# Kernel optimization log

Hardware: AMD Instinct MI355X
Metric: run time of the kernel (lower is better)

## Reference

```python
import jax, jax.numpy as jnp
import numpy as np

N, G, NPG = 51200, 512, 100
E, FA, FE = 300000, 64, 8
H, NH, DH, L, T = 256, 8, 32, 4, 5


def setup_inputs() -> dict:
    key = jax.random.key(0)
    it = iter(jax.random.split(key, 40))
    def rn(shape, s=0.05):
        return jax.random.normal(next(it), shape, jnp.float32) * s
    inp = {
        "x": rn((N, FA), 1.0),
        "edge_attr": rn((E, FE), 1.0),
        "edge_index": jax.random.randint(next(it), (2, E), 0, N),
        "batch": jnp.repeat(jnp.arange(G), NPG),
        "atom_w": rn((FA, H)), "atom_b": jnp.zeros((H,), jnp.float32),
        "edge_w": rn((FE, H)), "edge_b": jnp.zeros((H,), jnp.float32),
        "gat_lin_w": rn((L, H, H)), "gat_lin_edge_w": rn((L, H, H)),
        "gat_att_src": rn((L, NH, DH)), "gat_att_dst": rn((L, NH, DH)), "gat_att_edge": rn((L, NH, DH)),
        "gat_bias": jnp.zeros((L, H), jnp.float32),
        "bn_gamma": jnp.ones((L, H), jnp.float32), "bn_beta": jnp.zeros((L, H), jnp.float32),
        "mha_in_w": rn((3 * H, H)), "mha_in_b": jnp.zeros((3 * H,), jnp.float32),
        "mha_out_w": rn((H, H)), "mha_out_b": jnp.zeros((H,), jnp.float32),
        "sh_w1": rn((H, H)), "sh_b1": jnp.zeros((H,), jnp.float32),
        "sh_w2": rn((H, H // 2)), "sh_b2": jnp.zeros((H // 2,), jnp.float32),
        "head_w1": rn((T, H // 2, H // 4)), "head_b1": jnp.zeros((T, H // 4), jnp.float32),
        "head_w2": rn((T, H // 4, 1)), "head_b2": jnp.zeros((T, 1), jnp.float32),
    }
    return inp


def _forward(x, edge_attr, edge_index, batch, atom_w, atom_b, edge_w, edge_b,
             gat_lin_w, gat_lin_edge_w, gat_att_src, gat_att_dst, gat_att_edge,
             gat_bias, bn_gamma, bn_beta, mha_in_w, mha_in_b, mha_out_w, mha_out_b,
             sh_w1, sh_b1, sh_w2, sh_b2, head_w1, head_b1, head_w2, head_b2):
    src, dst = edge_index[0], edge_index[1]
    h = x @ atom_w + atom_b                      # [N, H] atom_encoder
    e = edge_attr @ edge_w + edge_b              # [E, H] edge_encoder
    # PyG GATConv add_self_loops=True, fill_value='mean' for edge_attr
    deg = jax.ops.segment_sum(jnp.ones((E,), e.dtype), dst, num_segments=N)
    e_self = jax.ops.segment_sum(e, dst, num_segments=N) / jnp.maximum(deg, 1.0)[:, None]
    loop = jnp.arange(N)
    src_f = jnp.concatenate([src, loop])
    dst_f = jnp.concatenate([dst, loop])
    e_f = jnp.concatenate([e, e_self], axis=0)   # [E+N, H]
    for i in range(L):
        res = h
        xs = (h @ gat_lin_w[i]).reshape(N, NH, DH)
        a_src = (xs * gat_att_src[i]).sum(-1)    # [N, NH]
        a_dst = (xs * gat_att_dst[i]).sum(-1)
        ee = (e_f @ gat_lin_edge_w[i]).reshape(-1, NH, DH)
        a_e = (ee * gat_att_edge[i]).sum(-1)     # [E+N, NH]
        alpha = jax.nn.leaky_relu(a_src[src_f] + a_dst[dst_f] + a_e, 0.2)
        mx = jax.ops.segment_max(alpha, dst_f, num_segments=N)   # segment softmax over dst
        ex = jnp.exp(alpha - mx[dst_f])
        den = jax.ops.segment_sum(ex, dst_f, num_segments=N)
        w = ex / (den[dst_f] + 1e-16)            # [E+N, NH]
        out = jax.ops.segment_sum(xs[src_f] * w[..., None], dst_f, num_segments=N)
        out = out.reshape(N, H) + gat_bias[i]
        mu = out.mean(0)
        var = out.var(0)                         # training-mode BatchNorm
        out = bn_gamma[i] * (out - mu) * jax.lax.rsqrt(var + 1e-5) + bn_beta[i]
        h = jax.nn.relu(out)
        if i > 0:
            h = h + res
    # per-graph MHA: graphs are fixed-size, so the ragged loop == batched attention
    xg = h.reshape(G, NPG, H)
    qkv = xg @ mha_in_w.T + mha_in_b             # [G, n, 3H]
    q, k, v = jnp.split(qkv, 3, axis=-1)
    def heads(t):
        return t.reshape(G, NPG, NH, DH).transpose(0, 2, 1, 3)
    q = heads(q) * (1.0 / np.sqrt(DH))
    k, v = heads(k), heads(v)
    att = jax.nn.softmax(jnp.einsum("ghnd,ghmd->ghnm", q, k), axis=-1)
    o = jnp.einsum("ghnm,ghmd->ghnd", att, v).transpose(0, 2, 1, 3).reshape(G, NPG, H)
    o = o @ mha_out_w.T + mha_out_b
    pooled = o.mean(1)                           # [G, H]
    s = jax.nn.relu(pooled @ sh_w1 + sh_b1)
    s = jax.nn.relu(s @ sh_w2 + sh_b2)           # [G, H//2]
    hh = jax.nn.relu(jnp.einsum("gd,tdk->gtk", s, head_w1) + head_b1)
    pred = jnp.einsum("gtk,tko->gto", hh, head_w2)[..., 0] + head_b2[:, 0]
    return pred                                  # [G, T]


def reference(x, edge_attr, edge_index, batch, atom_w, atom_b, edge_w, edge_b,
              gat_lin_w, gat_lin_edge_w, gat_att_src, gat_att_dst, gat_att_edge,
              gat_bias, bn_gamma, bn_beta, mha_in_w, mha_in_b, mha_out_w, mha_out_b,
              sh_w1, sh_b1, sh_w2, sh_b2, head_w1, head_b1, head_w2, head_b2):
    return _forward(x, edge_attr, edge_index, batch, atom_w, atom_b, edge_w, edge_b,
                    gat_lin_w, gat_lin_edge_w, gat_att_src, gat_att_dst, gat_att_edge,
                    gat_bias, bn_gamma, bn_beta, mha_in_w, mha_in_b, mha_out_w, mha_out_b,
                    sh_w1, sh_b1, sh_w2, sh_b2, head_w1, head_b1, head_w2, head_b2)
```

## Files before the change

### kernel.cpp

```cpp
#include <hip/hip_runtime.h>
#include <hip/hip_bf16.h>

#define N_NODES 51200
#define N_EDGES 300000
#define NFULL   351200
#define GRAPHS  512
#define NPGRAPH 100
#define FATOM   64
#define FEDGE   8
#define HDIM    256
#define NHEADS  8
#define DHEAD   32
#define LAYERS  4
#define TASKS   5
#define BN_SLOTS 16
#define SCAN_BLOCKS 50

typedef unsigned short u16;
typedef __attribute__((ext_vector_type(8))) short bf16x8;
typedef __attribute__((ext_vector_type(4))) float f32x4;

__device__ __forceinline__ float b2f(u16 u) {
    return __uint_as_float(((unsigned)u) << 16);
}
__device__ __forceinline__ u16 f2bf(float f) {
    unsigned u = __float_as_uint(f);
    unsigned r = u + 0x7fffu + ((u >> 16) & 1u);
    return (u16)(r >> 16);
}

__global__ __launch_bounds__(256)
void convert_kernel(const float* __restrict__ in, u16* __restrict__ out, int n) {
    int i = blockIdx.x * 256 + threadIdx.x;
    if (i < n) out[i] = f2bf(in[i]);
}

__global__ __launch_bounds__(256)
void convert_t_kernel(const float* __restrict__ in, u16* __restrict__ out, int R, int C) {
    int idx = blockIdx.x * 256 + threadIdx.x;
    if (idx >= R * C) return;
    int c = idx / R, r = idx % R;
    out[idx] = f2bf(in[(size_t)r * C + c]);
}

__global__ __launch_bounds__(256)
void convert_t4_kernel(const float* __restrict__ in, u16* __restrict__ out) {
    int idx = blockIdx.x * 256 + threadIdx.x;
    int li = idx >> 16, rem = idx & 65535;
    int c = rem >> 8, r = rem & 255;
    out[idx] = f2bf(in[(size_t)li * 65536 + r * 256 + c]);
}

template<bool BIAS, bool RELU>
__global__ __launch_bounds__(256, 2)
void gemm_mfma_kernel(const u16* __restrict__ A, const u16* __restrict__ Bt,
                      const float* __restrict__ bias, u16* __restrict__ C,
                      int M, int K, int N) {
    __shared__ u16 smem[136 * 128];
    u16* As = smem;
    u16* Bs = smem + 128 * 64;
    const int t = threadIdx.x;
    const int lane = t & 63;
    const int w = t >> 6;
    const int wr = w >> 1, wc = w & 1;

    const int nwg = (int)gridDim.x;
    const int bid = (int)blockIdx.x;
    const int q = nwg >> 3, r = nwg & 7;
    const int xcd = bid & 7, idx0 = bid >> 3;
    const int wgid = (xcd < r) ? xcd * (q + 1) + idx0
                               : r * (q + 1) + (xcd - r) * q + idx0;
    const int nx = N >> 7;
    const int bn = (wgid % nx) * 128;
    const int bm = (wgid / nx) * 128;

    f32x4 acc[4][4] = {};

    for (int kt = 0; kt < K; kt += 64) {
        uint4 ra[4], rb[4];
#pragma unroll
        for (int i = 0; i < 4; ++i) {
            int idx = i * 256 + t;
            int row = idx >> 3, ch = idx & 7;
            ra[i] = *(const uint4*)(A + (size_t)(bm + row) * K + kt + ch * 8);
            rb[i] = *(const uint4*)(Bt + (size_t)(bn + row) * K + kt + ch * 8);
        }
        __syncthreads();
#pragma unroll
        for (int i = 0; i < 4; ++i) {
            int idx = i * 256 + t;
            int row = idx >> 3, ch = idx & 7;
            int sw = ch ^ (row & 7);
            *(uint4*)((char*)As + row * 128 + sw * 16) = ra[i];
            *(uint4*)((char*)Bs + row * 128 + sw * 16) = rb[i];
        }
        __syncthreads();
#pragma unroll
        for (int kk = 0; kk < 2; ++kk) {
            bf16x8 af[4], bf[4];
#pragma unroll
            for (int m = 0; m < 4; ++m) {
                int rr = wr * 64 + m * 16 + (lane & 15);
                int ch = kk * 4 + (lane >> 4);
                af[m] = *(const bf16x8*)((const char*)As + rr * 128 + ((ch ^ (rr & 7)) << 4));
            }
#pragma unroll
            for (int n = 0; n < 4; ++n) {
                int rr = wc * 64 + n * 16 + (lane & 15);
                int ch = kk * 4 + (lane >> 4);
                bf[n] = *(const bf16x8*)((const char*)Bs + rr * 128 + ((ch ^ (rr & 7)) << 4));
            }
#pragma unroll
            for (int m = 0; m < 4; ++m)
#pragma unroll
                for (int n = 0; n < 4; ++n)
                    acc[m][n] = __builtin_amdgcn_mfma_f32_16x16x32_bf16(
                        af[m], bf[n], acc[m][n], 0, 0, 0);
        }
    }
    __syncthreads();
#pragma unroll
    for (int m = 0; m < 4; ++m)
#pragma unroll
        for (int n = 0; n < 4; ++n) {
            int coll = wc * 64 + n * 16 + (lane & 15);
            float bv = BIAS ? bias[bn + coll] : 0.f;
#pragma unroll
            for (int j = 0; j < 4; ++j) {
                float v = acc[m][n][j] + bv;
                if (RELU) v = fmaxf(v, 0.f);
                int rowl = wr * 64 + m * 16 + (lane >> 4) * 4 + j;
                smem[rowl * 136 + coll] = f2bf(v);
            }
        }
    __syncthreads();
#pragma unroll
    for (int p = 0; p < 8; ++p) {
        int rowl = p * 16 + (t >> 4);
        uint4 v = *(const uint4*)(smem + rowl * 136 + (t & 15) * 8);
        *(uint4*)(C + (size_t)(bm + rowl) * N + bn + (t & 15) * 8) = v;
    }
}

__global__ __launch_bounds__(256)
void edge_hist_kernel(const int* __restrict__ dst, int* __restrict__ deg) {
    int e = blockIdx.x * 256 + threadIdx.x;
    if (e >= N_EDGES) return;
    atomicAdd(&deg[dst[e]], 1);
}

__global__ __launch_bounds__(1024)
void scan1_kernel(const int* __restrict__ deg, int* __restrict__ row_ptr,
                  int* __restrict__ bsum) {
    __shared__ int buf[1024];
    const int b = blockIdx.x, t = threadIdx.x;
    const int i = b * 1024 + t;
    int v = deg[i] + 1;
    buf[t] = v;
    __syncthreads();
    for (int off = 1; off < 1024; off <<= 1) {
        int x = (t >= off) ? buf[t - off] : 0;
        __syncthreads();
        buf[t] += x;
        __syncthreads();
    }
    row_ptr[i] = buf[t] - v;
    if (t == 1023) bsum[b] = buf[t];
}

__global__ __launch_bounds__(64)
void scan2_kernel(int* __restrict__ bsum, int* __restrict__ row_ptr) {
    int t = threadIdx.x;
    int orig = (t < SCAN_BLOCKS) ? bsum[t] : 0;
    int v = orig;
    for (int off = 1; off < 64; off <<= 1) {
        int x = __shfl_up(v, off);
        if (t >= off) v += x;
    }
    if (t < SCAN_BLOCKS) bsum[t] = v - orig;
    if (t == SCAN_BLOCKS - 1) row_ptr[N_NODES] = v;
}

__global__ __launch_bounds__(256)
void scan3_kernel(int* __restrict__ row_ptr, const int* __restrict__ bsum) {
    int i = blockIdx.x * 256 + threadIdx.x;
    if (i >= N_NODES) return;
    row_ptr[i] += bsum[i >> 10];
}

__global__ __launch_bounds__(256)
void selfloop_init_kernel(const int* __restrict__ row_ptr, int* __restrict__ cursor,
                          int* __restrict__ col_src, int* __restrict__ col_eid) {
    int n = blockIdx.x * 256 + threadIdx.x;
    if (n >= N_NODES) return;
    cursor[n] = row_ptr[n];
    int pos = row_ptr[n + 1] - 1;
    col_src[pos] = n;
    col_eid[pos] = N_EDGES + n;
}

__global__ __launch_bounds__(256)
void scatter_kernel(const int* __restrict__ src, const int* __restrict__ dst,
                    int* __restrict__ cursor, int* __restrict__ col_src,
                    int* __restrict__ col_eid) {
    int e = blockIdx.x * 256 + threadIdx.x;
    if (e >= N_EDGES) return;
    int d = dst[e];
    int pos = atomicAdd(&cursor[d], 1);
    col_src[pos] = src[e];
    col_eid[pos] = e;
}

__global__ __launch_bounds__(256)
void proj_pe_kernel(const float* __restrict__ lin_edge_w, const float* __restrict__ att_edge,
                    float* __restrict__ P_e) {
    int idx = blockIdx.x * 256 + threadIdx.x;
    int li = idx >> 11;
    int rem = idx & 2047;
    int k = rem >> 3, nh = rem & 7;
    const float* w = lin_edge_w + (size_t)li * HDIM * HDIM + (size_t)k * HDIM + nh * DHEAD;
    const float* a = att_edge + li * HDIM + nh * DHEAD;
    float s = 0.f;
#pragma unroll
    for (int d = 0; d < DHEAD; ++d) s += w[d] * a[d];
    P_e[idx] = s;
}

__global__ __launch_bounds__(256)
void proj_q_kernel(const float* __restrict__ edge_w, const float* __restrict__ edge_b,
                   const float* __restrict__ P_e, float* __restrict__ Qm,
                   float* __restrict__ c0m) {
    int t = threadIdx.x;
    int li = t >> 6, f = (t >> 3) & 7, nh = t & 7;
    const float* pe = P_e + li * 2048;
    float q = 0.f;
    for (int k = 0; k < HDIM; ++k) q += edge_w[f * HDIM + k] * pe[k * 8 + nh];
    Qm[t] = q;
    if (t < 32) {
        int li2 = t >> 3, nh2 = t & 7;
        const float* pe2 = P_e + li2 * 2048;
        float c = 0.f;
        for (int k = 0; k < HDIM; ++k) c += edge_b[k] * pe2[k * 8 + nh2];
        c0m[t] = c;
    }
}

__global__ __launch_bounds__(256)
void ae_real_kernel(const float* __restrict__ edge_attr, const float* __restrict__ Qm,
                    const float* __restrict__ c0m, u16* __restrict__ a_e_all) {
    __shared__ float ea_s[8][8];
    __shared__ float Qs[256];
    __shared__ float c0s[32];
    const int t = threadIdx.x;
    const int e0 = blockIdx.x * 8;
    if (t < 64) ea_s[t >> 3][t & 7] = edge_attr[(size_t)e0 * 8 + t];
    Qs[t] = Qm[t];
    if (t < 32) c0s[t] = c0m[t];
    __syncthreads();
    int el = t >> 5, o = t & 31;
    int li = o >> 3, nh = o & 7;
    float v = c0s[o];
#pragma unroll
    for (int f = 0; f < 8; ++f) v += ea_s[el][f] * Qs[li * 64 + f * 8 + nh];
    a_e_all[(size_t)(e0 + el) * 32 + o] = f2bf(v);
}

__global__ __launch_bounds__(256)
void ae_self_kernel(const float* __restrict__ edge_attr, const int* __restrict__ row_ptr,
                    const int* __restrict__ col_eid, const float* __restrict__ Qm,
                    const float* __restrict__ c0m, u16* __restrict__ a_e_all) {
    __shared__ float ea_s[8][8];
    __shared__ int deg_s[8];
    __shared__ float Qs[256];
    __shared__ float c0s[32];
    const int t = threadIdx.x;
    const int n0 = blockIdx.x * 8;
    Qs[t] = Qm[t];
    if (t < 32) c0s[t] = c0m[t];
    if (t < 64) {
        int el = t >> 3, f = t & 7;
        int n = n0 + el;
        int s = row_ptr[n], e = row_ptr[n + 1] - 1;
        float acc = 0.f;
        for (int p = s; p < e; ++p)
            acc += edge_attr[(size_t)col_eid[p] * FEDGE + f];
        ea_s[el][f] = acc;
        if (f == 0) deg_s[el] = e - s;
    }
    __syncthreads();
    int el = t >> 5, o = t & 31;
    int li = o >> 3, nh = o & 7;
    int dg = deg_s[el];
    float v = 0.f;
    if (dg > 0) {
        float invd = 1.f / (float)dg;
        v = c0s[o];
#pragma unroll
        for (int f = 0; f < 8; ++f) v += ea_s[el][f] * invd * Qs[li * 64 + f * 8 + nh];
    }
    a_e_all[(size_t)(N_EDGES + n0 + el) * 32 + o] = f2bf(v);
}

__global__ __launch_bounds__(256)
void gat_asd_kernel(const u16* __restrict__ xs, const float* __restrict__ att_src_l,
                    const float* __restrict__ att_dst_l, float* __restrict__ a_src,
                    float* __restrict__ a_dst) {
    int node = (blockIdx.x << 2) + (threadIdx.x >> 6);
    int lane = threadIdx.x & 63;
    int c = lane << 2;
    ushort4 x4 = *(const ushort4*)(xs + (size_t)node * HDIM + c);
    float4 as4 = *(const float4*)(att_src_l + c);
    float4 ad4 = *(const float4*)(att_dst_l + c);
    float x0 = b2f(x4.x), x1 = b2f(x4.y), x2 = b2f(x4.z), x3 = b2f(x4.w);
    float vs = x0 * as4.x + x1 * as4.y + x2 * as4.z + x3 * as4.w;
    float vd = x0 * ad4.x + x1 * ad4.y + x2 * ad4.z + x3 * ad4.w;
#pragma unroll
    for (int off = 4; off >= 1; off >>= 1) {
        vs += __shfl_down(vs, off, 8);
        vd += __shfl_down(vd, off, 8);
    }
    if ((lane & 7) == 0) {
        a_src[node * 8 + (lane >> 3)] = vs;
        a_dst[node * 8 + (lane >> 3)] = vd;
    }
}

__global__ __launch_bounds__(256)
void gat_aggregate_kernel(const u16* __restrict__ xs, const float* __restrict__ a_src,
                          const float* __restrict__ a_dst, const u16* __restrict__ a_e_all,
                          const int* __restrict__ row_ptr, const int* __restrict__ col_src,
                          const int* __restrict__ col_eid, const float* __restrict__ bias_l,
                          u16* __restrict__ outb, int li) {
    int n = (blockIdx.x << 2) + (threadIdx.x >> 6);
    int lane = threadIdx.x & 63;
    int c = lane << 2;
    int nh = lane >> 3;
    const int aeo = li * 8 + nh;
    float adst = a_dst[n * 8 + nh];
    int s = row_ptr[n], e = row_ptr[n + 1];
    float4 acc = make_float4(0.f, 0.f, 0.f, 0.f);
    float den = 0.f;
    int p = s;
    for (; p + 4 <= e; p += 4) {
        int s0 = col_src[p],     s1 = col_src[p + 1];
        int s2 = col_src[p + 2], s3 = col_src[p + 3];
        int e0 = col_eid[p],     e1 = col_eid[p + 1];
        int e2 = col_eid[p + 2], e3 = col_eid[p + 3];
        float as0 = a_src[s0 * 8 + nh], as1 = a_src[s1 * 8 + nh];
        float as2 = a_src[s2 * 8 + nh], as3 = a_src[s3 * 8 + nh];
        float ae0 = b2f(a_e_all[(size_t)e0 * 32 + aeo]);
        float ae1 = b2f(a_e_all[(size_t)e1 * 32 + aeo]);
        float ae2 = b2f(a_e_all[(size_t)e2 * 32 + aeo]);
        float ae3 = b2f(a_e_all[(size_t)e3 * 32 + aeo]);
        ushort4 x0 = *(const ushort4*)(xs + (size_t)s0 * HDIM + c);
        ushort4 x1 = *(const ushort4*)(xs + (size_t)s1 * HDIM + c);
        ushort4 x2 = *(const ushort4*)(xs + (size_t)s2 * HDIM + c);
        ushort4 x3 = *(const ushort4*)(xs + (size_t)s3 * HDIM + c);
        float al0 = as0 + adst + ae0; al0 = (al0 > 0.f) ? al0 : 0.2f * al0;
        float al1 = as1 + adst + ae1; al1 = (al1 > 0.f) ? al1 : 0.2f * al1;
        float al2 = as2 + adst + ae2; al2 = (al2 > 0.f) ? al2 : 0.2f * al2;
        float al3 = as3 + adst + ae3; al3 = (al3 > 0.f) ? al3 : 0.2f * al3;
        float ex0 = __expf(al0), ex1 = __expf(al1);
        float ex2 = __expf(al2), ex3 = __expf(al3);
        den += (ex0 + ex1) + (ex2 + ex3);
        acc.x += ex0 * b2f(x0.x) + ex1 * b2f(x1.x) + ex2 * b2f(x2.x) + ex3 * b2f(x3.x);
        acc.y += ex0 * b2f(x0.y) + ex1 * b2f(x1.y) + ex2 * b2f(x2.y) + ex3 * b2f(x3.y);
        acc.z += ex0 * b2f(x0.z) + ex1 * b2f(x1.z) + ex2 * b2f(x2.z) + ex3 * b2f(x3.z);
        acc.w += ex0 * b2f(x0.w) + ex1 * b2f(x1.w) + ex2 * b2f(x2.w) + ex3 * b2f(x3.w);
    }
    for (; p + 2 <= e; p += 2) {
        int s0 = col_src[p],     s1 = col_src[p + 1];
        int e0 = col_eid[p],     e1 = col_eid[p + 1];
        float as0 = a_src[s0 * 8 + nh];
        float as1 = a_src[s1 * 8 + nh];
        float ae0 = b2f(a_e_all[(size_t)e0 * 32 + aeo]);
        float ae1 = b2f(a_e_all[(size_t)e1 * 32 + aeo]);
        ushort4 x0 = *(const ushort4*)(xs + (size_t)s0 * HDIM + c);
        ushort4 x1 = *(const ushort4*)(xs + (size_t)s1 * HDIM + c);
        float al0 = as0 + adst + ae0; al0 = (al0 > 0.f) ? al0 : 0.2f * al0;
        float al1 = as1 + adst + ae1; al1 = (al1 > 0.f) ? al1 : 0.2f * al1;
        float ex0 = __expf(al0);
        float ex1 = __expf(al1);
        den += ex0 + ex1;
        acc.x += ex0 * b2f(x0.x) + ex1 * b2f(x1.x);
        acc.y += ex0 * b2f(x0.y) + ex1 * b2f(x1.y);
        acc.z += ex0 * b2f(x0.z) + ex1 * b2f(x1.z);
        acc.w += ex0 * b2f(x0.w) + ex1 * b2f(x1.w);
    }
    if (p < e) {
        int s0 = col_src[p];
        int e0 = col_eid[p];
        float al = a_src[s0 * 8 + nh] + adst + b2f(a_e_all[(size_t)e0 * 32 + aeo]);
        al = (al > 0.f) ? al : 0.2f * al;
        float ex = __expf(al);
        den += ex;
        ushort4 x4 = *(const ushort4*)(xs + (size_t)s0 * HDIM + c);
        acc.x += ex * b2f(x4.x); acc.y += ex * b2f(x4.y);
        acc.z += ex * b2f(x4.z); acc.w += ex * b2f(x4.w);
    }
    float inv = 1.f / (den + 1e-16f);
    float4 b4 = *(const float4*)(bias_l + c);
    ushort4 o4;
    o4.x = f2bf(acc.x * inv + b4.x);
    o4.y = f2bf(acc.y * inv + b4.y);
    o4.z = f2bf(acc.z * inv + b4.z);
    o4.w = f2bf(acc.w * inv + b4.w);
    *(ushort4*)(outb + (size_t)n * HDIM + c) = o4;
}

__global__ __launch_bounds__(256)
void bn_stats1_kernel(const u16* __restrict__ outb, float* __restrict__ gsum,
                      float* __restrict__ gsq) {
    __shared__ float lsum[8][HDIM];
    __shared__ float lsq[8][HDIM];
    const int t = threadIdx.x;
    const int b = blockIdx.x;
    const int c0 = (t & 31) * 8;
    const int g = t >> 5;
    const size_t base = (size_t)b * 64 * HDIM;
    float s[8] = {}, q[8] = {};
#pragma unroll
    for (int i = 0; i < 8; ++i) {
        const u16* p = outb + base + i * 2048 + t * 8;
        ushort4 u0 = *(const ushort4*)p;
        ushort4 u1 = *(const ushort4*)(p + 4);
        float v0 = b2f(u0.x), v1 = b2f(u0.y), v2 = b2f(u0.z), v3 = b2f(u0.w);
        float v4 = b2f(u1.x), v5 = b2f(u1.y), v6 = b2f(u1.z), v7 = b2f(u1.w);
        s[0] += v0; q[0] += v0 * v0;  s[1] += v1; q[1] += v1 * v1;
        s[2] += v2; q[2] += v2 * v2;  s[3] += v3; q[3] += v3 * v3;
        s[4] += v4; q[4] += v4 * v4;  s[5] += v5; q[5] += v5 * v5;
        s[6] += v6; q[6] += v6 * v6;  s[7] += v7; q[7] += v7 * v7;
    }
#pragma unroll
    for (int j = 0; j < 8; ++j) { lsum[g][c0 + j] = s[j]; lsq[g][c0 + j] = q[j]; }
    __syncthreads();
    float ts = 0.f, tq = 0.f;
#pragma unroll
    for (int gg = 0; gg < 8; ++gg) { ts += lsum[gg][t]; tq += lsq[gg][t]; }
    int slot = b & (BN_SLOTS - 1);
    atomicAdd(&gsum[slot * HDIM + t], ts);
    atomicAdd(&gsq[slot * HDIM + t], tq);
}

__global__ __launch_bounds__(256)
void bn_stats2_kernel(float* __restrict__ gsum, float* __restrict__ gsq,
                      float* __restrict__ mu, float* __restrict__ inv) {
    int c = threadIdx.x;
    float s = 0.f, s2 = 0.f;
#pragma unroll
    for (int b = 0; b < BN_SLOTS; ++b) {
        s += gsum[b * HDIM + c];
        s2 += gsq[b * HDIM + c];
        gsum[b * HDIM + c] = 0.f;
        gsq[b * HDIM + c] = 0.f;
    }
    float m = s / (float)N_NODES;
    float var = s2 / (float)N_NODES - m * m;
    mu[c] = m;
    inv[c] = rsqrtf(var + 1e-5f);
}

__global__ __launch_bounds__(256)
void bn_apply_kernel(const u16* __restrict__ outb, const float* __restrict__ mu,
                     const float* __restrict__ inv, const float* __restrict__ gamma_l,
                     const float* __restrict__ beta_l, u16* __restrict__ h, int addres) {
    int idx = blockIdx.x * 256 + threadIdx.x;
    int c = (idx & 63) << 2;
    ushort4 v4 = *(const ushort4*)(outb + (size_t)idx * 4);
    float4 m4 = *(const float4*)(mu + c);
    float4 i4 = *(const float4*)(inv + c);
    float4 g4 = *(const float4*)(gamma_l + c);
    float4 b4 = *(const float4*)(beta_l + c);
    float v0 = fmaxf(g4.x * (b2f(v4.x) - m4.x) * i4.x + b4.x, 0.f);
    float v1 = fmaxf(g4.y * (b2f(v4.y) - m4.y) * i4.y + b4.y, 0.f);
    float v2 = fmaxf(g4.z * (b2f(v4.z) - m4.z) * i4.z + b4.z, 0.f);
    float v3 = fmaxf(g4.w * (b2f(v4.w) - m4.w) * i4.w + b4.w, 0.f);
    if (addres) {
        ushort4 h4 = *(const ushort4*)(h + (size_t)idx * 4);
        v0 += b2f(h4.x); v1 += b2f(h4.y); v2 += b2f(h4.z); v3 += b2f(h4.w);
    }
    ushort4 o4;
    o4.x = f2bf(v0); o4.y = f2bf(v1); o4.z = f2bf(v2); o4.w = f2bf(v3);
    *(ushort4*)(h + (size_t)idx * 4) = o4;
}

__global__ __launch_bounds__(64)
void mha_attn_kernel(const u16* __restrict__ qkv, u16* __restrict__ o) {
    const int g = blockIdx.x >> 3;
    const int head = blockIdx.x & 7;
    const int l = threadIdx.x;
    __shared__ u16 VT[DHEAD][132];
    __shared__ u16 P[16][132];
    const size_t base = (size_t)g * NPGRAPH * 768 + head * 32;

    for (int idx = l; idx < 32 * 128; idx += 64) {
        int m = idx >> 5, d = idx & 31;
        u16 v = 0;
        if (m < 100) v = qkv[base + (size_t)m * 768 + 512 + d];
        VT[d][m] = v;
    }
    bf16x8 kf[7];
#pragma unroll
    for (int n = 0; n < 7; ++n) {
        int r = n * 16 + (l & 15);
        kf[n] = *(const bf16x8*)(qkv + base + (size_t)r * 768 + 256 + ((l >> 4) << 3));
    }
    __syncthreads();
    bf16x8 vf[2][4];
#pragma unroll
    for (int dt = 0; dt < 2; ++dt)
#pragma unroll
        for (int kc = 0; kc < 4; ++kc)
            vf[dt][kc] = *(const bf16x8*)(&VT[dt * 16 + (l & 15)][kc * 32 + ((l >> 4) << 3)]);

    const float SC = 0.17677669529663687f;
    const bool c6ok = (96 + (l & 15)) < 100;

    for (int mt = 0; mt < 7; ++mt) {
        int qr = mt * 16 + (l & 15);
        bf16x8 qf = *(const bf16x8*)(qkv + base + (size_t)qr * 768 + ((l >> 4) << 3));
        f32x4 sa[7];
#pragma unroll
        for (int n = 0; n < 7; ++n) {
            f32x4 z = {0.f, 0.f, 0.f, 0.f};
            sa[n] = __builtin_amdgcn_mfma_f32_16x16x32_bf16(qf, kf[n], z, 0, 0, 0);
        }
        float linv[4];
#pragma unroll
        for (int j = 0; j < 4; ++j) {
            float m = -1e30f;
#pragma unroll
            for (int n = 0; n < 6; ++n) m = fmaxf(m, sa[n][j]);
            if (c6ok) m = fmaxf(m, sa[6][j]);
            m *= SC;
#pragma unroll
            for (int off = 1; off < 16; off <<= 1) m = fmaxf(m, __shfl_xor(m, off));
            float ls = 0.f;
            float pv[7];
#pragma unroll
            for (int n = 0; n < 7; ++n) {
                float p_ = 0.f;
                if (n < 6 || c6ok) p_ = __expf(SC * sa[n][j] - m);
                pv[n] = p_;
                ls += p_;
            }
#pragma unroll
            for (int off = 1; off < 16; off <<= 1) ls += __shfl_xor(ls, off);
            linv[j] = 1.f / ls;
            int rt = ((l >> 4) << 2) + j;
#pragma unroll
            for (int n = 0; n < 7; ++n) P[rt][n * 16 + (l & 15)] = f2bf(pv[n]);
            P[rt][112 + (l & 15)] = 0;
        }
        __syncthreads();
        f32x4 oa[2] = {};
#pragma unroll
        for (int kc = 0; kc < 4; ++kc) {
            bf16x8 pf = *(const bf16x8*)(&P[l & 15][kc * 32 + ((l >> 4) << 3)]);
            oa[0] = __builtin_amdgcn_mfma_f32_16x16x32_bf16(pf, vf[0][kc], oa[0], 0, 0, 0);
            oa[1] = __builtin_amdgcn_mfma_f32_16x16x32_bf16(pf, vf[1][kc], oa[1], 0, 0, 0);
        }
        int r0 = mt * 16 + ((l >> 4) << 2);
#pragma unroll
        for (int dt = 0; dt < 2; ++dt)
#pragma unroll
            for (int j = 0; j < 4; ++j) {
                int r = r0 + j;
                if (r < 100)
                    o[(size_t)(g * NPGRAPH + r) * HDIM + head * 32 + dt * 16 + (l & 15)] =
                        f2bf(oa[dt][j] * linv[j]);
            }
        __syncthreads();
    }
}

__global__ __launch_bounds__(256)
void pool_kernel(const u16* __restrict__ o2, u16* __restrict__ pooled) {
    int g = blockIdx.x;
    int c = threadIdx.x;
    float s = 0.f;
    for (int r = 0; r < NPGRAPH; ++r) s += b2f(o2[((size_t)g * NPGRAPH + r) * HDIM + c]);
    pooled[g * HDIM + c] = f2bf(s * 0.01f);
}

__global__ __launch_bounds__(64)
void heads_kernel(const u16* __restrict__ s2, const float* __restrict__ w1,
                  const float* __restrict__ b1, const float* __restrict__ w2,
                  const float* __restrict__ b2, float* __restrict__ out) {
    int g = blockIdx.x / TASKS;
    int tt = blockIdx.x % TASKS;
    int d = threadIdx.x;
    float s = b1[tt * 64 + d];
    const u16* srow = s2 + (size_t)g * 128;
    const float* wcol = w1 + (size_t)tt * 128 * 64 + d;
    for (int k = 0; k < 128; ++k) s += b2f(srow[k]) * wcol[k * 64];
    s = fmaxf(s, 0.f);
    float v = s * w2[tt * 64 + d];
#pragma unroll
    for (int off = 32; off >= 1; off >>= 1) v += __shfl_down(v, off);
    if (d == 0) out[g * TASKS + tt] = v + b2[tt];
}

extern "C" void kernel_launch(void* const* d_in, const int* in_sizes, int n_in,
                              void* d_out, int out_size, void* d_ws, size_t ws_size,
                              hipStream_t stream) {
    const float* x          = (const float*)d_in[0];
    const float* edge_attr  = (const float*)d_in[1];
    const int*   edge_index = (const int*)d_in[2];
    const float* atom_w     = (const float*)d_in[4];
    const float* atom_b     = (const float*)d_in[5];
    const float* edge_w     = (const float*)d_in[6];
    const float* edge_b     = (const float*)d_in[7];
    const float* gat_lin_w  = (const float*)d_in[8];
    const float* gat_lin_ew = (const float*)d_in[9];
    const float* att_src    = (const float*)d_in[10];
    const float* att_dst    = (const float*)d_in[11];
    const float* att_edge   = (const float*)d_in[12];
    const float* gat_bias   = (const float*)d_in[13];
    const float* bn_gamma   = (const float*)d_in[14];
    const float* bn_beta    = (const float*)d_in[15];
    const float* mha_in_w   = (const float*)d_in[16];
    const float* mha_in_b   = (const float*)d_in[17];
    const float* mha_out_w  = (const float*)d_in[18];
    const float* mha_out_b  = (const float*)d_in[19];
    const float* sh_w1      = (const float*)d_in[20];
    const float* sh_b1      = (const float*)d_in[21];
    const float* sh_w2      = (const float*)d_in[22];
    const float* sh_b2      = (const float*)d_in[23];
    const float* head_w1    = (const float*)d_in[24];
    const float* head_b1    = (const float*)d_in[25];
    const float* head_w2    = (const float*)d_in[26];
    const float* head_b2    = (const float*)d_in[27];
    float* out = (float*)d_out;

    const int* src = edge_index;
    const int* dst = edge_index + N_EDGES;

    size_t off = 0;
    auto alloc = [&](size_t bytes) -> void* {
        void* p = (char*)d_ws + off;
        off += (bytes + 255) & ~(size_t)255;
        return p;
    };
    const size_t NHB = (size_t)N_NODES * HDIM * sizeof(u16);
    u16* h_buf = (u16*)alloc(NHB);
    char* region1 = (char*)alloc((size_t)N_NODES * 768 * sizeof(u16));
    u16* xs_buf  = (u16*)region1;
    u16* out_buf = (u16*)(region1 + NHB);
    u16* a_e_all = (u16*)(region1 + 2 * NHB);
    u16* qkv_buf = (u16*)region1;
    u16* o2_buf  = (u16*)region1;
    u16* o_buf   = h_buf;
    u16* x_bf    = out_buf;
    float* a_src_b = (float*)alloc((size_t)N_NODES * 8 * sizeof(float));
    float* a_dst_b = (float*)alloc((size_t)N_NODES * 8 * sizeof(float));
    float* gsum    = (float*)alloc(BN_SLOTS * HDIM * sizeof(float));
    float* gsq     = (float*)alloc(BN_SLOTS * HDIM * sizeof(float));
    float* mu_b    = (float*)alloc(HDIM * sizeof(float));
    float* inv_b   = (float*)alloc(HDIM * sizeof(float));
    float* P_e     = (float*)alloc(LAYERS * HDIM * 8 * sizeof(float));
    float* Qm      = (float*)alloc(256 * sizeof(float));
    float* c0m     = (float*)alloc(32 * sizeof(float));
    u16* atom_wt   = (u16*)alloc((size_t)HDIM * FATOM * sizeof(u16));
    u16* lin_wt    = (u16*)alloc((size_t)LAYERS * HDIM * HDIM * sizeof(u16));
    u16* in_w_bf   = (u16*)alloc((size_t)768 * HDIM * sizeof(u16));
    u16* out_w_bf  = (u16*)alloc((size_t)HDIM * HDIM * sizeof(u16));
    u16* sh1_t     = (u16*)alloc((size_t)HDIM * HDIM * sizeof(u16));
    u16* sh2_t     = (u16*)alloc((size_t)128 * HDIM * sizeof(u16));
    u16* pooled    = (u16*)alloc((size_t)GRAPHS * HDIM * sizeof(u16));
    u16* s1_b      = (u16*)alloc((size_t)GRAPHS * HDIM * sizeof(u16));
    u16* s2_b      = (u16*)alloc((size_t)GRAPHS * 128 * sizeof(u16));
    int* deg       = (int*)alloc(N_NODES * sizeof(int));
    int* row_ptr   = (int*)alloc((N_NODES + 256) * sizeof(int));
    int* cursor    = (int*)alloc(N_NODES * sizeof(int));
    int* col_src   = (int*)alloc(NFULL * sizeof(int));
    int* col_eid   = (int*)alloc(NFULL * sizeof(int));
    int* bsum      = (int*)alloc(64 * sizeof(int));
    (void)ws_size; (void)in_sizes; (void)n_in; (void)out_size;

    convert_t_kernel<<<(HDIM * FATOM + 255) / 256, 256, 0, stream>>>(atom_w, atom_wt, FATOM, HDIM);
    convert_t4_kernel<<<(LAYERS * HDIM * HDIM) / 256, 256, 0, stream>>>(gat_lin_w, lin_wt);
    convert_kernel<<<(768 * HDIM + 255) / 256, 256, 0, stream>>>(mha_in_w, in_w_bf, 768 * HDIM);
    convert_kernel<<<(HDIM * HDIM + 255) / 256, 256, 0, stream>>>(mha_out_w, out_w_bf, HDIM * HDIM);
    convert_t_kernel<<<(HDIM * HDIM + 255) / 256, 256, 0, stream>>>(sh_w1, sh1_t, HDIM, HDIM);
    convert_t_kernel<<<(HDIM * 128 + 255) / 256, 256, 0, stream>>>(sh_w2, sh2_t, HDIM, 128);
    convert_kernel<<<(N_NODES * FATOM + 255) / 256, 256, 0, stream>>>(x, x_bf, N_NODES * FATOM);

    hipMemsetAsync(deg, 0, N_NODES * sizeof(int), stream);
    edge_hist_kernel<<<(N_EDGES + 255) / 256, 256, 0, stream>>>(dst, deg);
    scan1_kernel<<<SCAN_BLOCKS, 1024, 0, stream>>>(deg, row_ptr, bsum);
    scan2_kernel<<<1, 64, 0, stream>>>(bsum, row_ptr);
    scan3_kernel<<<N_NODES / 256, 256, 0, stream>>>(row_ptr, bsum);
    selfloop_init_kernel<<<(N_NODES + 255) / 256, 256, 0, stream>>>(row_ptr, cursor, col_src, col_eid);
    scatter_kernel<<<(N_EDGES + 255) / 256, 256, 0, stream>>>(src, dst, cursor, col_src, col_eid);

    proj_pe_kernel<<<32, 256, 0, stream>>>(gat_lin_ew, att_edge, P_e);
    proj_q_kernel<<<1, 256, 0, stream>>>(edge_w, edge_b, P_e, Qm, c0m);
    ae_real_kernel<<<N_EDGES / 8, 256, 0, stream>>>(edge_attr, Qm, c0m, a_e_all);
    ae_self_kernel<<<N_NODES / 8, 256, 0, stream>>>(
        edge_attr, row_ptr, col_eid, Qm, c0m, a_e_all);

    gemm_mfma_kernel<true, false><<<(HDIM / 128) * (N_NODES / 128), 256, 0, stream>>>(
        x_bf, atom_wt, atom_b, h_buf, N_NODES, FATOM, HDIM);

    hipMemsetAsync(gsum, 0, BN_SLOTS * HDIM * sizeof(float), stream);
    hipMemsetAsync(gsq, 0, BN_SLOTS * HDIM * sizeof(float), stream);
    for (int li = 0; li < LAYERS; ++li) {
        gemm_mfma_kernel<false, false><<<(HDIM / 128) * (N_NODES / 128), 256, 0, stream>>>(
            h_buf, lin_wt + (size_t)li * HDIM * HDIM, nullptr, xs_buf, N_NODES, HDIM, HDIM);
        gat_asd_kernel<<<N_NODES / 4, 256, 0, stream>>>(
            xs_buf, att_src + li * HDIM, att_dst + li * HDIM, a_src_b, a_dst_b);
        gat_aggregate_kernel<<<N_NODES / 4, 256, 0, stream>>>(
            xs_buf, a_src_b, a_dst_b, a_e_all, row_ptr, col_src, col_eid,
            gat_bias + li * HDIM, out_buf, li);
        bn_stats1_kernel<<<N_NODES / 64, 256, 0, stream>>>(out_buf, gsum, gsq);
        bn_stats2_kernel<<<1, 256, 0, stream>>>(gsum, gsq, mu_b, inv_b);
        bn_apply_kernel<<<(N_NODES * HDIM / 4) / 256, 256, 0, stream>>>(
            out_buf, mu_b, inv_b, bn_gamma + li * HDIM, bn_beta + li * HDIM, h_buf, li > 0 ? 1 : 0);
    }

    gemm_mfma_kernel<true, false><<<(768 / 128) * (N_NODES / 128), 256, 0, stream>>>(
        h_buf, in_w_bf, mha_in_b, qkv_buf, N_NODES, HDIM, 768);
    mha_attn_kernel<<<GRAPHS * NHEADS, 64, 0, stream>>>(qkv_buf, o_buf);
    gemm_mfma_kernel<true, false><<<(HDIM / 128) * (N_NODES / 128), 256, 0, stream>>>(
        o_buf, out_w_bf, mha_out_b, o2_buf, N_NODES, HDIM, HDIM);
    pool_kernel<<<GRAPHS, 256, 0, stream>>>(o2_buf, pooled);

    gemm_mfma_kernel<true, true><<<(HDIM / 128) * (GRAPHS / 128), 256, 0, stream>>>(
        pooled, sh1_t, sh_b1, s1_b, GRAPHS, HDIM, HDIM);
    gemm_mfma_kernel<true, true><<<(128 / 128) * (GRAPHS / 128), 256, 0, stream>>>(
        s1_b, sh2_t, sh_b2, s2_b, GRAPHS, HDIM, 128);
    heads_kernel<<<GRAPHS * TASKS, 64, 0, stream>>>(
        s2_b, head_w1, head_b1, head_w2, head_b2, out);
}
```

Before: 871.0 us.

## Fuse GAT attention-score dot products into GEMM epilogue and split QKV projection

```diff
diff --git a/kernel.cpp b/kernel.cpp
--- a/kernel.cpp
+++ b/kernel.cpp
@@ -51,11 +51,13 @@
     out[idx] = f2bf(in[(size_t)li * 65536 + r * 256 + c]);
 }
 
-template<bool BIAS, bool RELU>
+template<bool BIAS, bool RELU, bool ASD>
 __global__ __launch_bounds__(256, 2)
 void gemm_mfma_kernel(const u16* __restrict__ A, const u16* __restrict__ Bt,
                       const float* __restrict__ bias, u16* __restrict__ C,
-                      int M, int K, int N) {
+                      int M, int K, int N,
+                      const float* __restrict__ att_s, const float* __restrict__ att_d,
+                      float* __restrict__ a_src, float* __restrict__ a_dst) {
     __shared__ u16 smem[136 * 128];
     u16* As = smem;
     u16* Bs = smem + 128 * 64;
@@ -118,6 +120,41 @@
                         af[m], bf[n], acc[m][n], 0, 0, 0);
         }
     }
+
+    if (ASD) {
+        float as_[4], ad_[4];
+#pragma unroll
+        for (int n = 0; n < 4; ++n) {
+            int col = bn + wc * 64 + n * 16 + (lane & 15);
+            as_[n] = att_s[col];
+            ad_[n] = att_d[col];
+        }
+        const int h0 = (bn >> 5) + wc * 2;
+#pragma unroll
+        for (int m = 0; m < 4; ++m)
+#pragma unroll
+            for (int j = 0; j < 4; ++j) {
+                float s0 = acc[m][0][j] * as_[0] + acc[m][1][j] * as_[1];
+                float s1 = acc[m][2][j] * as_[2] + acc[m][3][j] * as_[3];
+                float d0 = acc[m][0][j] * ad_[0] + acc[m][1][j] * ad_[1];
+                float d1 = acc[m][2][j] * ad_[2] + acc[m][3][j] * ad_[3];
+#pragma unroll
+                for (int off = 1; off < 16; off <<= 1) {
+                    s0 += __shfl_xor(s0, off);
+                    s1 += __shfl_xor(s1, off);
+                    d0 += __shfl_xor(d0, off);
+                    d1 += __shfl_xor(d1, off);
+                }
+                if ((lane & 15) == 0) {
+                    int node = bm + wr * 64 + m * 16 + (lane >> 4) * 4 + j;
+                    a_src[node * 8 + h0]     = s0;
+                    a_src[node * 8 + h0 + 1] = s1;
+                    a_dst[node * 8 + h0]     = d0;
+                    a_dst[node * 8 + h0 + 1] = d1;
+                }
+            }
+    }
+
     __syncthreads();
 #pragma unroll
     for (int m = 0; m < 4; ++m)
@@ -299,30 +336,6 @@
         for (int f = 0; f < 8; ++f) v += ea_s[el][f] * invd * Qs[li * 64 + f * 8 + nh];
     }
     a_e_all[(size_t)(N_EDGES + n0 + el) * 32 + o] = f2bf(v);
-}
-
-__global__ __launch_bounds__(256)
-void gat_asd_kernel(const u16* __restrict__ xs, const float* __restrict__ att_src_l,
-                    const float* __restrict__ att_dst_l, float* __restrict__ a_src,
-                    float* __restrict__ a_dst) {
-    int node = (blockIdx.x << 2) + (threadIdx.x >> 6);
-    int lane = threadIdx.x & 63;
-    int c = lane << 2;
-    ushort4 x4 = *(const ushort4*)(xs + (size_t)node * HDIM + c);
-    float4 as4 = *(const float4*)(att_src_l + c);
-    float4 ad4 = *(const float4*)(att_dst_l + c);
-    float x0 = b2f(x4.x), x1 = b2f(x4.y), x2 = b2f(x4.z), x3 = b2f(x4.w);
-    float vs = x0 * as4.x + x1 * as4.y + x2 * as4.z + x3 * as4.w;
-    float vd = x0 * ad4.x + x1 * ad4.y + x2 * ad4.z + x3 * ad4.w;
-#pragma unroll
-    for (int off = 4; off >= 1; off >>= 1) {
-        vs += __shfl_down(vs, off, 8);
-        vd += __shfl_down(vd, off, 8);
-    }
-    if ((lane & 7) == 0) {
-        a_src[node * 8 + (lane >> 3)] = vs;
-        a_dst[node * 8 + (lane >> 3)] = vd;
-    }
 }
 
 __global__ __launch_bounds__(256)
@@ -485,25 +498,26 @@
 }
 
 __global__ __launch_bounds__(64)
-void mha_attn_kernel(const u16* __restrict__ qkv, u16* __restrict__ o) {
+void mha_attn_kernel(const u16* __restrict__ Qb, const u16* __restrict__ Kb,
+                     const u16* __restrict__ Vb, u16* __restrict__ o) {
     const int g = blockIdx.x >> 3;
     const int head = blockIdx.x & 7;
     const int l = threadIdx.x;
     __shared__ u16 VT[DHEAD][132];
     __shared__ u16 P[16][132];
-    const size_t base = (size_t)g * NPGRAPH * 768 + head * 32;
+    const size_t base = (size_t)g * NPGRAPH * HDIM + head * 32;
 
     for (int idx = l; idx < 32 * 128; idx += 64) {
         int m = idx >> 5, d = idx & 31;
         u16 v = 0;
-        if (m < 100) v = qkv[base + (size_t)m * 768 + 512 + d];
+        if (m < 100) v = Vb[base + (size_t)m * HDIM + d];
         VT[d][m] = v;
     }
     bf16x8 kf[7];
 #pragma unroll
     for (int n = 0; n < 7; ++n) {
         int r = n * 16 + (l & 15);
-        kf[n] = *(const bf16x8*)(qkv + base + (size_t)r * 768 + 256 + ((l >> 4) << 3));
+        kf[n] = *(const bf16x8*)(Kb + base + (size_t)r * HDIM + ((l >> 4) << 3));
     }
     __syncthreads();
     bf16x8 vf[2][4];
@@ -518,7 +532,7 @@
 
     for (int mt = 0; mt < 7; ++mt) {
         int qr = mt * 16 + (l & 15);
-        bf16x8 qf = *(const bf16x8*)(qkv + base + (size_t)qr * 768 + ((l >> 4) << 3));
+        bf16x8 qf = *(const bf16x8*)(Qb + base + (size_t)qr * HDIM + ((l >> 4) << 3));
         f32x4 sa[7];
 #pragma unroll
         for (int n = 0; n < 7; ++n) {
@@ -648,7 +662,9 @@
     u16* xs_buf  = (u16*)region1;
     u16* out_buf = (u16*)(region1 + NHB);
     u16* a_e_all = (u16*)(region1 + 2 * NHB);
-    u16* qkv_buf = (u16*)region1;
+    u16* q_buf   = (u16*)region1;
+    u16* k_buf   = (u16*)(region1 + NHB);
+    u16* v_buf   = (u16*)(region1 + 2 * NHB);
     u16* o2_buf  = (u16*)region1;
     u16* o_buf   = h_buf;
     u16* x_bf    = out_buf;
@@ -700,16 +716,16 @@
     ae_self_kernel<<<N_NODES / 8, 256, 0, stream>>>(
         edge_attr, row_ptr, col_eid, Qm, c0m, a_e_all);
 
-    gemm_mfma_kernel<true, false><<<(HDIM / 128) * (N_NODES / 128), 256, 0, stream>>>(
-        x_bf, atom_wt, atom_b, h_buf, N_NODES, FATOM, HDIM);
+    gemm_mfma_kernel<true, false, false><<<(HDIM / 128) * (N_NODES / 128), 256, 0, stream>>>(
+        x_bf, atom_wt, atom_b, h_buf, N_NODES, FATOM, HDIM,
+        nullptr, nullptr, nullptr, nullptr);
 
     hipMemsetAsync(gsum, 0, BN_SLOTS * HDIM * sizeof(float), stream);
     hipMemsetAsync(gsq, 0, BN_SLOTS * HDIM * sizeof(float), stream);
     for (int li = 0; li < LAYERS; ++li) {
-        gemm_mfma_kernel<false, false><<<(HDIM / 128) * (N_NODES / 128), 256, 0, stream>>>(
-            h_buf, lin_wt + (size_t)li * HDIM * HDIM, nullptr, xs_buf, N_NODES, HDIM, HDIM);
-        gat_asd_kernel<<<N_NODES / 4, 256, 0, stream>>>(
-            xs_buf, att_src + li * HDIM, att_dst + li * HDIM, a_src_b, a_dst_b);
+        gemm_mfma_kernel<false, false, true><<<(HDIM / 128) * (N_NODES / 128), 256, 0, stream>>>(
+            h_buf, lin_wt + (size_t)li * HDIM * HDIM, nullptr, xs_buf, N_NODES, HDIM, HDIM,
+            att_src + li * HDIM, att_dst + li * HDIM, a_src_b, a_dst_b);
         gat_aggregate_kernel<<<N_NODES / 4, 256, 0, stream>>>(
             xs_buf, a_src_b, a_dst_b, a_e_all, row_ptr, col_src, col_eid,
             gat_bias + li * HDIM, out_buf, li);
@@ -719,17 +735,27 @@
             out_buf, mu_b, inv_b, bn_gamma + li * HDIM, bn_beta + li * HDIM, h_buf, li > 0 ? 1 : 0);
     }
 
-    gemm_mfma_kernel<true, false><<<(768 / 128) * (N_NODES / 128), 256, 0, stream>>>(
-        h_buf, in_w_bf, mha_in_b, qkv_buf, N_NODES, HDIM, 768);
-    mha_attn_kernel<<<GRAPHS * NHEADS, 64, 0, stream>>>(qkv_buf, o_buf);
-    gemm_mfma_kernel<true, false><<<(HDIM / 128) * (N_NODES / 128), 256, 0, stream>>>(
-        o_buf, out_w_bf, mha_out_b, o2_buf, N_NODES, HDIM, HDIM);
+    gemm_mfma_kernel<true, false, false><<<(HDIM / 128) * (N_NODES / 128), 256, 0, stream>>>(
+        h_buf, in_w_bf, mha_in_b, q_buf, N_NODES, HDIM, HDIM,
+        nullptr, nullptr, nullptr, nullptr);
+    gemm_mfma_kernel<true, false, false><<<(HDIM / 128) * (N_NODES / 128), 256, 0, stream>>>(
+        h_buf, in_w_bf + (size_t)256 * HDIM, mha_in_b + 256, k_buf, N_NODES, HDIM, HDIM,
+        nullptr, nullptr, nullptr, nullptr);
+    gemm_mfma_kernel<true, false, false><<<(HDIM / 128) * (N_NODES / 128), 256, 0, stream>>>(
+        h_buf, in_w_bf + (size_t)512 * HDIM, mha_in_b + 512, v_buf, N_NODES, HDIM, HDIM,
+        nullptr, nullptr, nullptr, nullptr);
+    mha_attn_kernel<<<GRAPHS * NHEADS, 64, 0, stream>>>(q_buf, k_buf, v_buf, o_buf);
+    gemm_mfma_kernel<true, false, false><<<(HDIM / 128) * (N_NODES / 128), 256, 0, stream>>>(
+        o_buf, out_w_bf, mha_out_b, o2_buf, N_NODES, HDIM, HDIM,
+        nullptr, nullptr, nullptr, nullptr);
     pool_kernel<<<GRAPHS, 256, 0, stream>>>(o2_buf, pooled);
 
-    gemm_mfma_kernel<true, true><<<(HDIM / 128) * (GRAPHS / 128), 256, 0, stream>>>(
-        pooled, sh1_t, sh_b1, s1_b, GRAPHS, HDIM, HDIM);
-    gemm_mfma_kernel<true, true><<<(128 / 128) * (GRAPHS / 128), 256, 0, stream>>>(
-        s1_b, sh2_t, sh_b2, s2_b, GRAPHS, HDIM, 128);
+    gemm_mfma_kernel<true, true, false><<<(HDIM / 128) * (GRAPHS / 128), 256, 0, stream>>>(
+        pooled, sh1_t, sh_b1, s1_b, GRAPHS, HDIM, HDIM,
+        nullptr, nullptr, nullptr, nullptr);
+    gemm_mfma_kernel<true, true, false><<<(128 / 128) * (GRAPHS / 128), 256, 0, stream>>>(
+        s1_b, sh2_t, sh_b2, s2_b, GRAPHS, HDIM, 128,
+        nullptr, nullptr, nullptr, nullptr);
     heads_kernel<<<GRAPHS * TASKS, 64, 0, stream>>>(
         s2_b, head_w1, head_b1, head_w2, head_b2, out);
 }
```

Measured after the change: 891.8 us. 1.02x slower.
